# Optimization experiments

Measured on AMD Instinct MI355X. Metric: run time of the kernel, lower is better.

The kernel has to match this reference:

```python
import jax, jax.numpy as jnp
import numpy as np

E = 131072
MS, MV = 64, 32            # node/edge/out irreps: 64x0e + 32x1o (dim 160)
DIM = MS + 3 * MV
SC = 64                    # edge scalar dim
BETA = 1.6791767           # normalize2mom(silu) constant used by e3nn FullyConnectedNet
SQ3 = np.float32(np.sqrt(3.0))


def _split(x, ms, mv):
    # e3nn layout: [mul_s scalars | mul_v vectors (mul-major, xyz-minor)]
    return x[:, :ms], x[:, ms:].reshape(x.shape[0], mv, 3)


def _tp(xs, xv, ys, yv, Wss, Wvv, Wsv, Wvs):
    # uvw fully-connected tensor product of (m1s x0e + m1v x1o) with (1x0e + 1x1o),
    # component irrep normalization, 1/sqrt(fan_in) path weights.
    m1s, m1v = xs.shape[1], xv.shape[1]
    s_a = jnp.einsum('eu,uw->ew', xs * ys, Wss) / np.sqrt(m1s)              # 0e x 0e -> 0e
    dot = jnp.einsum('eui,ei->eu', xv, yv) / SQ3                            # 1o x 1o -> 0e
    s_b = jnp.einsum('eu,uw->ew', dot, Wvv) / np.sqrt(m1v)
    v_a = jnp.einsum('eu,ei,uw->ewi', xs, yv, Wsv) / np.sqrt(m1s)           # 0e x 1o -> 1o
    v_b = jnp.einsum('eui,uw->ewi', xv * ys[:, :, None], Wvs) / np.sqrt(m1v)  # 1o x 0e -> 1o
    return jnp.concatenate([s_a, s_b], 1), jnp.concatenate([v_a, v_b], 1)


def _mlp(x, W1, W2, W3):
    # e3nn FullyConnectedNet with silu: variance-preserving layers
    h = BETA * jax.nn.silu(x @ W1 / np.sqrt(W1.shape[0]))
    h = BETA * jax.nn.silu(h @ W2 / np.sqrt(W2.shape[0]))
    return h @ W3 / np.sqrt(W3.shape[0])


def _scale_linear(ms_, mv_, w, Wls, Wlv):
    # LinearScaleWithWeights: per-channel (uvu) scale by generated weights, then o3.Linear
    nS = ms_.shape[1]
    s = ms_ * w[:, :nS]
    v = mv_ * w[:, nS:, None]
    s2 = s @ Wls / np.sqrt(Wls.shape[0])
    v2 = jnp.einsum('eui,uw->ewi', v, Wlv) / np.sqrt(Wlv.shape[0])
    return s2, v2


def _linear(s, v, Ws, Wv):
    return s @ Ws / np.sqrt(Ws.shape[0]), jnp.einsum('eui,uw->ewi', v, Wv) / np.sqrt(Wv.shape[0])


def setup_inputs() -> dict:
    key = jax.random.key(0)
    ks = jax.random.split(key, 32)
    r = lambda i, shp: jax.random.normal(ks[i], shp, dtype=jnp.float32)
    return {
        'node_feats_src': r(0, (E, DIM)),
        'node_feats_dst': r(1, (E, DIM)),
        'edge_feats':     r(2, (E, DIM)),
        'local_env_edge': r(3, (E, 4)),
        'edge_scalars':   r(4, (E, SC)),
        # node TP (combined 128x0e+64x1o x 1x0e+1x1o -> 128x0e+64x1o)
        'Wn_ss': r(5, (2 * MS, MS)), 'Wn_vv': r(6, (2 * MV, MS)),
        'Wn_sv': r(7, (2 * MS, MV)), 'Wn_vs': r(8, (2 * MV, MV)),
        # edge TP (64x0e+32x1o x 1x0e+1x1o -> 128x0e+64x1o)
        'We_ss': r(9, (MS, MS)), 'We_vv': r(10, (MV, MS)),
        'We_sv': r(11, (MS, MV)), 'We_vs': r(12, (MV, MV)),
        # scaler output linears (128x0e+64x1o -> 64x0e+32x1o)
        'Wns_s': r(13, (2 * MS, MS)), 'Wns_v': r(14, (2 * MV, MV)),
        'Wes_s': r(15, (2 * MS, MS)), 'Wes_v': r(16, (2 * MV, MV)),
        # final output linears (irreps_out -> irreps_out)
        'Wno_s': r(17, (MS, MS)), 'Wno_v': r(18, (MV, MV)),
        'Weo_s': r(19, (MS, MS)), 'Weo_v': r(20, (MV, MV)),
        # radial MLPs [64,64,64,192]
        'Wnm1': r(21, (SC, 64)), 'Wnm2': r(22, (64, 64)), 'Wnm3': r(23, (64, 2 * MS + 2 * MV)),
        'Wem1': r(24, (SC, 64)), 'Wem2': r(25, (64, 64)), 'Wem3': r(26, (64, 2 * MS + 2 * MV)),
    }


def reference(node_feats_src, node_feats_dst, edge_feats, local_env_edge, edge_scalars,
              Wn_ss, Wn_vv, Wn_sv, Wn_vs, We_ss, We_vv, We_sv, We_vs,
              Wns_s, Wns_v, Wes_s, Wes_v, Wno_s, Wno_v, Weo_s, Weo_v,
              Wnm1, Wnm2, Wnm3, Wem1, Wem2, Wem3):
    ss, sv = _split(node_feats_src, MS, MV)
    ds, dv = _split(node_feats_dst, MS, MV)
    # AttentionHeadsToVector over stack([src,dst]): per-irrep concat -> 128x0e + 64x1o
    xs = jnp.concatenate([ss, ds], 1)
    xv = jnp.concatenate([sv, dv], 1)
    ys = local_env_edge[:, :1]
    yv = local_env_edge[:, 1:4]
    # node branch
    w_n = _mlp(edge_scalars, Wnm1, Wnm2, Wnm3)
    m_s, m_v = _tp(xs, xv, ys, yv, Wn_ss, Wn_vv, Wn_sv, Wn_vs)
    n_s, n_v = _scale_linear(m_s, m_v, w_n, Wns_s, Wns_v)
    # edge branch
    w_e = _mlp(edge_scalars, Wem1, Wem2, Wem3)
    es, ev = _split(edge_feats, MS, MV)
    e_ms, e_mv = _tp(es, ev, ys, yv, We_ss, We_vv, We_sv, We_vs)
    e_s, e_v = _scale_linear(e_ms, e_mv, w_e, Wes_s, Wes_v)
    # final linears + sum
    on_s, on_v = _linear(n_s, n_v, Wno_s, Wno_v)
    oe_s, oe_v = _linear(e_s, e_v, Weo_s, Weo_v)
    out_s = on_s + oe_s
    out_v = on_v + oe_v
    return jnp.concatenate([out_s, out_v.reshape(out_v.shape[0], -1)], 1)
```

## Files before the change

kernel.cpp:

```cpp
#include <hip/hip_runtime.h>


typedef short  bf16x8 __attribute__((ext_vector_type(8)));
typedef float  f32x4  __attribute__((ext_vector_type(4)));

#define FENCE() asm volatile("" ::: "memory")

constexpr float BETA  = 1.6791767f;
constexpr float RS128 = 0.088388347648318447f;
constexpr float RS64  = 0.125f;
constexpr float RS32  = 0.176776695296636881f;
constexpr float RSQ3  = 0.577350269189625842f;

enum : int {
  O_nm1 = 0,      O_nm2 = 4096,   O_nm3 = 8192,
  O_em1 = 20480,  O_em2 = 24576,  O_em3 = 28672,
  O_nss = 40960,  O_nsv = 49152,  O_nvv = 53248,  O_nvs = 57344,
  O_ess = 59392,  O_esv = 63488,  O_evv = 65536,  O_evs = 67584,
  O_cns = 68608,  O_cnv = 76800,  O_ces = 78848,  O_cev = 87040,
  W_TOTAL = 89088
};

enum : int { ST = 260, H0n = 0, H0e = 64, H1n = 128, H1e = 192, MSP = 0, MV = 128 };

struct Ptrs {
  const float *src, *dst, *ef, *env, *scal;
  const ushort* wf;
  float *out;
};

struct PrepArgs {
  const float* src[14];
  int K[14], N[14], ofs[14];
  ushort* dst;
};
struct Prep2Args {
  const float* A[4]; const float* B[4];
  int K[4], N[4], inner[4], ofs[4];
  float scale[4];
  ushort* dst;
};

__device__ __forceinline__ ushort f2b(float x) {
  union { float f; unsigned u; } v; v.f = x;
  unsigned r = v.u + 0x7fffu + ((v.u >> 16) & 1u);
  return (ushort)(r >> 16);
}
__device__ __forceinline__ unsigned pk2(float a, float b) {
  unsigned r;
  asm("v_cvt_pk_bf16_f32 %0, %1, %2" : "=v"(r) : "v"(a), "v"(b));
  return r;
}
__device__ __forceinline__ float plo(unsigned p) {
  union { unsigned u; float f; } v; v.u = p << 16; return v.f;
}
__device__ __forceinline__ float phi(unsigned p) {
  union { unsigned u; float f; } v; v.u = p & 0xffff0000u; return v.f;
}

__global__ __launch_bounds__(256) void prep_kernel(PrepArgs A) {
  const int mat = blockIdx.x;
  const float* __restrict__ src = A.src[mat];
  const int K = A.K[mat], N = A.N[mat], KS = K >> 5;
  ushort* dst = A.dst + A.ofs[mat];
  const int total = (N * K) >> 3;
  for (int gi = threadIdx.x; gi < total; gi += 256) {
    int t = gi / (64 * KS), r = gi - t * 64 * KS;
    int ks = r >> 6, lane = r & 63;
    int cc = lane & 15, gg = lane >> 4;
    int n = t * 16 + cc, k0 = ks * 32 + gg * 8;
    ushort v[8];
#pragma unroll
    for (int j = 0; j < 8; ++j) v[j] = f2b(src[(size_t)(k0 + j) * N + n]);
    *(uint4*)(dst + (size_t)gi * 8) = *(const uint4*)v;
  }
}

__global__ __launch_bounds__(256) void prep2_kernel(Prep2Args Z) {
  const int m = blockIdx.x;
  const float* __restrict__ A = Z.A[m];
  const float* __restrict__ B = Z.B[m];
  const int K = Z.K[m], N = Z.N[m], I = Z.inner[m], KS = K >> 5;
  const float sc = Z.scale[m];
  ushort* dst = Z.dst + Z.ofs[m];

  __shared__ float sAt[8192];
  __shared__ float sB [4096];
  for (int idx = threadIdx.x; idx < K * I; idx += 256) {
    int k = idx / I, u = idx - k * I;
    sAt[u * K + k] = A[idx];
  }
  for (int idx = threadIdx.x; idx < I * N; idx += 256) sB[idx] = B[idx];
  __syncthreads();

  const int total = (N * K) >> 3;
  for (int gi = blockIdx.y * 256 + threadIdx.x; gi < total; gi += gridDim.y * 256) {
    int t = gi / (64 * KS), r = gi - t * 64 * KS;
    int ks = r >> 6, lane = r & 63;
    int cc = lane & 15, gg = lane >> 4;
    int n = t * 16 + cc, k0 = ks * 32 + gg * 8;
    float acc[8] = {0, 0, 0, 0, 0, 0, 0, 0};
    for (int u = 0; u < I; ++u) {
      float bv = sB[u * N + n];
      const float* ap = &sAt[u * K + k0];
#pragma unroll
      for (int j = 0; j < 8; ++j) acc[j] += ap[j] * bv;
    }
    ushort v[8];
#pragma unroll
    for (int j = 0; j < 8; ++j) v[j] = f2b(acc[j] * sc);
    *(uint4*)(dst + (size_t)gi * 8) = *(const uint4*)v;
  }
}

template<int N>
__device__ __forceinline__ void lda(const ushort* __restrict__ wb, unsigned lofs, bf16x8* a) {
#pragma unroll
  for (int i = 0; i < N; ++i) a[i] = *(const bf16x8*)(wb + i * 512 + lofs);
}
template<int T, int KS>
__device__ __forceinline__ void mfm(const bf16x8* a, const bf16x8* bf, f32x4* out) {
#pragma unroll
  for (int t = 0; t < T; ++t) {
    f32x4 acc = (f32x4){0, 0, 0, 0};
#pragma unroll
    for (int ks = 0; ks < KS; ++ks)
      acc = __builtin_amdgcn_mfma_f32_16x16x32_bf16(a[t * KS + ks], bf[ks], acc, 0, 0, 0);
    out[t] = acc;
  }
}
template<int T, int KS>
__device__ __forceinline__ void mfmacc(const bf16x8* a, const bf16x8* bf, f32x4* out) {
#pragma unroll
  for (int t = 0; t < T; ++t)
#pragma unroll
    for (int ks = 0; ks < KS; ++ks)
      out[t] = __builtin_amdgcn_mfma_f32_16x16x32_bf16(a[t * KS + ks], bf[ks], out[t], 0, 0, 0);
}

__device__ __forceinline__ void put2(ushort* b, int cg, int col, const f32x4& d) {
  uint2 p; p.x = pk2(d[0], d[1]); p.y = pk2(d[2], d[3]);
  *(uint2*)(b + cg + col) = p;
}
__device__ __forceinline__ bf16x8 getf(const ushort* b, int cg, int col, int g) {
  return *(const bf16x8*)(b + cg + col + 8 * g);
}
__device__ __forceinline__ bf16x8 ldf8(const float* __restrict__ p) {
  float4 a = *(const float4*)p, b4 = *(const float4*)(p + 4);
  union { unsigned u[4]; bf16x8 v; } r;
  r.u[0] = pk2(a.x, a.y); r.u[1] = pk2(a.z, a.w);
  r.u[2] = pk2(b4.x, b4.y); r.u[3] = pk2(b4.z, b4.w);
  return r.v;
}
__device__ __forceinline__ f32x4 silu4(const f32x4& d) {
  f32x4 o;
#pragma unroll
  for (int r = 0; r < 4; ++r) { float z = d[r] * 0.125f; o[r] = BETA * z / (1.f + __expf(-z)); }
  return o;
}
__device__ __forceinline__ void vecwin(const float* __restrict__ p,
                                       float y0, float y1, float y2,
                                       bf16x8& dotf, bf16x8* xvf) {
  float v[24];
#pragma unroll
  for (int q = 0; q < 6; ++q) *(float4*)&v[4 * q] = *(const float4*)(p + 4 * q);
  float dj[8];
#pragma unroll
  for (int j = 0; j < 8; ++j)
    dj[j] = (v[3 * j] * y0 + v[3 * j + 1] * y1 + v[3 * j + 2] * y2) * RSQ3;
  union { unsigned u[4]; bf16x8 w; } t;
#pragma unroll
  for (int q = 0; q < 4; ++q) t.u[q] = pk2(dj[2 * q], dj[2 * q + 1]);
  dotf = t.w;
#pragma unroll
  for (int i = 0; i < 3; ++i) {
#pragma unroll
    for (int q = 0; q < 4; ++q) t.u[q] = pk2(v[6 * q + i], v[6 * q + 3 + i]);
    xvf[i] = t.w;
  }
}

__device__ __forceinline__ void mlp3(const ushort* __restrict__ wb, unsigned lofs,
                                     const bf16x8* h2, uint2* Wp) {
  bf16x8 aa[6], ab[6];
  lda<6>(wb, lofs, aa);
  lda<6>(wb + 6 * 512, lofs, ab);
  f32x4 dw[3];
  mfm<3, 2>(aa, h2, dw);
  lda<6>(wb + 12 * 512, lofs, aa);
#pragma unroll
  for (int t = 0; t < 3; ++t) { Wp[t].x = pk2(dw[t][0]*0.125f, dw[t][1]*0.125f); Wp[t].y = pk2(dw[t][2]*0.125f, dw[t][3]*0.125f); }
  mfm<3, 2>(ab, h2, dw);
  lda<6>(wb + 18 * 512, lofs, ab);
#pragma unroll
  for (int t = 0; t < 3; ++t) { Wp[3+t].x = pk2(dw[t][0]*0.125f, dw[t][1]*0.125f); Wp[3+t].y = pk2(dw[t][2]*0.125f, dw[t][3]*0.125f); }
  mfm<3, 2>(aa, h2, dw);
#pragma unroll
  for (int t = 0; t < 3; ++t) { Wp[6+t].x = pk2(dw[t][0]*0.125f, dw[t][1]*0.125f); Wp[6+t].y = pk2(dw[t][2]*0.125f, dw[t][3]*0.125f); }
  mfm<3, 2>(ab, h2, dw);
#pragma unroll
  for (int t = 0; t < 3; ++t) { Wp[9+t].x = pk2(dw[t][0]*0.125f, dw[t][1]*0.125f); Wp[9+t].y = pk2(dw[t][2]*0.125f, dw[t][3]*0.125f); }
}

template<bool ED, bool ACC>
__device__ __forceinline__ void tp_sl(
    const ushort* __restrict__ WF, ushort* bA, int cg, int g, unsigned lofs,
    const bf16x8* xsf, const bf16x8* dotf, const bf16x8* xvi,
    const uint2* Wp, float ys, float yv0, float yv1, float yv2,
    f32x4* os, f32x4 (*ov)[2]) {
  constexpr int KA = ED ? 2 : 4;
  constexpr int KB = ED ? 1 : 2;
  const float SA = ED ? RS64 : RS128;
  const float SB = ED ? RS32 : RS64;

  {
    bf16x8 a[4 * KA]; f32x4 d[4];
    lda<4 * KA>(WF + (ED ? O_ess : O_nss), lofs, a);
    mfm<4, KA>(a, xsf, d);
#pragma unroll
    for (int t = 0; t < 4; ++t) {
      f32x4 m;
      m[0] = d[t][0]*ys*SA*plo(Wp[t].x); m[1] = d[t][1]*ys*SA*phi(Wp[t].x);
      m[2] = d[t][2]*ys*SA*plo(Wp[t].y); m[3] = d[t][3]*ys*SA*phi(Wp[t].y);
      put2(bA, cg, MSP + 16 * t + 4 * g, m);
    }
  }
  {
    bf16x8 a[4 * KB]; f32x4 d[4];
    lda<4 * KB>(WF + (ED ? O_evv : O_nvv), lofs, a);
    mfm<4, KB>(a, dotf, d);
#pragma unroll
    for (int t = 0; t < 4; ++t) {
      f32x4 m;
      m[0] = d[t][0]*SB*plo(Wp[4+t].x); m[1] = d[t][1]*SB*phi(Wp[4+t].x);
      m[2] = d[t][2]*SB*plo(Wp[4+t].y); m[3] = d[t][3]*SB*phi(Wp[4+t].y);
      put2(bA, cg, MSP + 64 + 16 * t + 4 * g, m);
    }
  }
  FENCE();
  bf16x8 mpf[4];
#pragma unroll
  for (int ks = 0; ks < 4; ++ks) mpf[ks] = getf(bA, cg, MSP + 32 * ks, g);
  bf16x8 acs[16];
  lda<16>(WF + (ED ? O_ces : O_cns), lofs, acs);

  f32x4 ga[2];
  {
    bf16x8 a[2 * KA];
    lda<2 * KA>(WF + (ED ? O_esv : O_nsv), lofs, a);
    mfm<2, KA>(a, xsf, ga);
  }
  bf16x8 avs[2 * KB];
  lda<2 * KB>(WF + (ED ? O_evs : O_nvs), lofs, avs);
  bf16x8 acv[4];
  lda<4>(WF + (ED ? O_cev : O_cnv), lofs, acv);
#pragma unroll
  for (int i = 0; i < 3; ++i) {
    f32x4 db[2];
    mfm<2, KB>(avs, xvi + i * KB, db);
    float yvi = (i == 0) ? yv0 : ((i == 1) ? yv1 : yv2);
#pragma unroll
    for (int t = 0; t < 2; ++t) {
      f32x4 m;
      m[0] = ga[t][0]*SA*yvi*plo(Wp[8+t].x); m[1] = ga[t][1]*SA*yvi*phi(Wp[8+t].x);
      m[2] = ga[t][2]*SA*yvi*plo(Wp[8+t].y); m[3] = ga[t][3]*SA*yvi*phi(Wp[8+t].y);
      put2(bA, cg, MV + 16 * t + 4 * g, m);
    }
#pragma unroll
    for (int t = 0; t < 2; ++t) {
      f32x4 m;
      m[0] = db[t][0]*ys*SB*plo(Wp[10+t].x); m[1] = db[t][1]*ys*SB*phi(Wp[10+t].x);
      m[2] = db[t][2]*ys*SB*plo(Wp[10+t].y); m[3] = db[t][3]*ys*SB*phi(Wp[10+t].y);
      put2(bA, cg, MV + 32 + 16 * t + 4 * g, m);
    }
    FENCE();
    bf16x8 mvf[2] = { getf(bA, cg, MV, g), getf(bA, cg, MV + 32, g) };
    if (ACC) mfmacc<2, 2>(acv, mvf, ov[i]);
    else     mfm<2, 2>(acv, mvf, ov[i]);
    FENCE();
  }
  if (ACC) mfmacc<4, 4>(acs, mpf, os);
  else     mfm<4, 4>(acs, mpf, os);
}

__global__ __launch_bounds__(64, 2) void mp_kernel(Ptrs P) {
  const int lane = threadIdx.x & 63;
  const int c    = lane & 15, g  = lane >> 4;
  const unsigned lofs = lane * 8;
  const int cg   = c * ST;
  const int e    = blockIdx.x * 16 + c;
  const ushort* __restrict__ WF = P.wf;

  __shared__ ushort sb[16][ST];
  ushort* bA = &sb[0][0];

  const float* __restrict__ rs = P.src + (size_t)e * 160;
  const float* __restrict__ rd = P.dst + (size_t)e * 160;
  const float* __restrict__ re = P.ef  + (size_t)e * 160;
  const float* __restrict__ rq = P.scal + (size_t)e * 64;

  bf16x8 a1n[8], a1e[8];
  lda<8>(WF + O_nm1, lofs, a1n);
  lda<8>(WF + O_em1, lofs, a1e);

  float4 ev = *(const float4*)(P.env + (size_t)e * 4);
  const float ys = ev.x, yv0 = ev.y, yv1 = ev.z, yv2 = ev.w;
  bf16x8 sc[2];
  sc[0] = ldf8(rq + 8 * g);
  sc[1] = ldf8(rq + 32 + 8 * g);

  {
    f32x4 dn[4], de[4];
    mfm<4, 2>(a1n, sc, dn); mfm<4, 2>(a1e, sc, de);
#pragma unroll
    for (int t = 0; t < 4; ++t) put2(bA, cg, H0n + 16 * t + 4 * g, silu4(dn[t]));
#pragma unroll
    for (int t = 0; t < 4; ++t) put2(bA, cg, H0e + 16 * t + 4 * g, silu4(de[t]));
  }
  FENCE();

  bf16x8 a2n[8], a2e[8];
  lda<8>(WF + O_nm2, lofs, a2n);
  lda<8>(WF + O_em2, lofs, a2e);
  bf16x8 xsf_n[4];
  xsf_n[0] = ldf8(rs + 8 * g);  xsf_n[1] = ldf8(rs + 32 + 8 * g);
  xsf_n[2] = ldf8(rd + 8 * g);  xsf_n[3] = ldf8(rd + 32 + 8 * g);
  bf16x8 dot_n[2], xv_n[6];
  {
    bf16x8 tmp[3];
    vecwin(rs + 64 + 24 * g, yv0, yv1, yv2, dot_n[0], tmp);
    xv_n[0] = tmp[0]; xv_n[2] = tmp[1]; xv_n[4] = tmp[2];
    vecwin(rd + 64 + 24 * g, yv0, yv1, yv2, dot_n[1], tmp);
    xv_n[1] = tmp[0]; xv_n[3] = tmp[1]; xv_n[5] = tmp[2];
  }
  {
    bf16x8 hn[2] = { getf(bA, cg, H0n, g), getf(bA, cg, H0n + 32, g) };
    bf16x8 he[2] = { getf(bA, cg, H0e, g), getf(bA, cg, H0e + 32, g) };
    f32x4 dn[4], de[4];
    mfm<4, 2>(a2n, hn, dn); mfm<4, 2>(a2e, he, de);
#pragma unroll
    for (int t = 0; t < 4; ++t) put2(bA, cg, H1n + 16 * t + 4 * g, silu4(dn[t]));
#pragma unroll
    for (int t = 0; t < 4; ++t) put2(bA, cg, H1e + 16 * t + 4 * g, silu4(de[t]));
  }
  FENCE();

  uint2 Wpn[12];
  {
    bf16x8 h2n[2] = { getf(bA, cg, H1n, g), getf(bA, cg, H1n + 32, g) };
    mlp3(WF + O_nm3, lofs, h2n, Wpn);
  }
  FENCE();

  f32x4 os[4]; f32x4 ov[3][2];
  tp_sl<false, false>(WF, bA, cg, g, lofs, xsf_n, dot_n, xv_n, Wpn, ys, yv0, yv1, yv2, os, ov);

  bf16x8 xsf_e[2], dot_e[1], xv_e[3];
  xsf_e[0] = ldf8(re + 8 * g); xsf_e[1] = ldf8(re + 32 + 8 * g);
  {
    bf16x8 tmp[3];
    vecwin(re + 64 + 24 * g, yv0, yv1, yv2, dot_e[0], tmp);
    xv_e[0] = tmp[0]; xv_e[1] = tmp[1]; xv_e[2] = tmp[2];
  }
  uint2 Wpe[12];
  {
    bf16x8 h2e[2] = { getf(bA, cg, H1e, g), getf(bA, cg, H1e + 32, g) };
    mlp3(WF + O_em3, lofs, h2e, Wpe);
  }
  FENCE();

  tp_sl<true, true>(WF, bA, cg, g, lofs, xsf_e, dot_e, xv_e, Wpe, ys, yv0, yv1, yv2, os, ov);

  float* __restrict__ po = P.out + (size_t)e * 160;
#pragma unroll
  for (int t = 0; t < 4; ++t) {
    float4 o = { os[t][0], os[t][1], os[t][2], os[t][3] };
    *(float4*)(po + 16 * t + 4 * g) = o;
  }
#pragma unroll
  for (int t = 0; t < 2; ++t) {
    float vv[12];
#pragma unroll
    for (int r = 0; r < 4; ++r)
#pragma unroll
      for (int i = 0; i < 3; ++i) vv[3 * r + i] = ov[i][t][r];
    *(float4*)(po + 64 + 48 * t + 12 * g)     = *(float4*)&vv[0];
    *(float4*)(po + 64 + 48 * t + 12 * g + 4) = *(float4*)&vv[4];
    *(float4*)(po + 64 + 48 * t + 12 * g + 8) = *(float4*)&vv[8];
  }
}

extern "C" void kernel_launch(void* const* d_in, const int* in_sizes, int n_in,
                              void* d_out, int out_size, void* d_ws, size_t ws_size,
                              hipStream_t stream) {
  PrepArgs A;
  const int src_idx[14] = {21,22,23, 24,25,26, 5,7,6,8, 9,11,10,12};
  const int Ks[14] = {64,64,64, 64,64,64, 128,128,64,64, 64,64,32,32};
  const int Ns[14] = {64,64,192, 64,64,192, 64,32,64,32, 64,32,64,32};
  const int Os[14] = {O_nm1,O_nm2,O_nm3, O_em1,O_em2,O_em3,
                      O_nss,O_nsv,O_nvv,O_nvs, O_ess,O_esv,O_evv,O_evs};
  for (int i = 0; i < 14; ++i) {
    A.src[i] = (const float*)d_in[src_idx[i]];
    A.K[i] = Ks[i]; A.N[i] = Ns[i]; A.ofs[i] = Os[i];
  }
  A.dst = (ushort*)d_ws;
  prep_kernel<<<dim3(14), dim3(256), 0, stream>>>(A);

  Prep2Args Z;
  Z.A[0] = (const float*)d_in[13]; Z.B[0] = (const float*)d_in[17];
  Z.K[0] = 128; Z.N[0] = 64; Z.inner[0] = 64; Z.ofs[0] = O_cns; Z.scale[0] = RS128 * RS64;
  Z.A[1] = (const float*)d_in[14]; Z.B[1] = (const float*)d_in[18];
  Z.K[1] = 64;  Z.N[1] = 32; Z.inner[1] = 32; Z.ofs[1] = O_cnv; Z.scale[1] = RS64 * RS32;
  Z.A[2] = (const float*)d_in[15]; Z.B[2] = (const float*)d_in[19];
  Z.K[2] = 128; Z.N[2] = 64; Z.inner[2] = 64; Z.ofs[2] = O_ces; Z.scale[2] = RS128 * RS64;
  Z.A[3] = (const float*)d_in[16]; Z.B[3] = (const float*)d_in[20];
  Z.K[3] = 64;  Z.N[3] = 32; Z.inner[3] = 32; Z.ofs[3] = O_cev; Z.scale[3] = RS64 * RS32;
  Z.dst = (ushort*)d_ws;
  prep2_kernel<<<dim3(4, 4), dim3(256), 0, stream>>>(Z);

  Ptrs P;
  P.src  = (const float*)d_in[0];
  P.dst  = (const float*)d_in[1];
  P.ef   = (const float*)d_in[2];
  P.env  = (const float*)d_in[3];
  P.scal = (const float*)d_in[4];
  P.wf   = (const ushort*)d_ws;
  P.out  = (float*)d_out;

  const int E = in_sizes[0] / 160;
  mp_kernel<<<dim3(E / 16), dim3(64), 0, stream>>>(P);
}
```

Measured before the change: 148.6 us.

## Process two 16-edge tiles per wave to reuse weight fragments

Each 64-lane wavefront now handles 32 edges as two 16-edge tiles, A and B. Every weight fragment loaded for the MLP layers, tensor products and final linears is applied to both tiles, which halves weight-load traffic per edge. The shared buffer doubles to 32 rows and the grid halves. Some loads are split into halves to limit register pressure, but keeping two sets of accumulators and inputs live still raises register use, which risks spills or lower occupancy.

```diff
diff --git a/kernel.cpp b/kernel.cpp
--- a/kernel.cpp
+++ b/kernel.cpp
@@ -180,75 +180,84 @@
   }
 }
 
-__device__ __forceinline__ void mlp3(const ushort* __restrict__ wb, unsigned lofs,
-                                     const bf16x8* h2, uint2* Wp) {
-  bf16x8 aa[6], ab[6];
-  lda<6>(wb, lofs, aa);
-  lda<6>(wb + 6 * 512, lofs, ab);
-  f32x4 dw[3];
-  mfm<3, 2>(aa, h2, dw);
-  lda<6>(wb + 12 * 512, lofs, aa);
-#pragma unroll
-  for (int t = 0; t < 3; ++t) { Wp[t].x = pk2(dw[t][0]*0.125f, dw[t][1]*0.125f); Wp[t].y = pk2(dw[t][2]*0.125f, dw[t][3]*0.125f); }
-  mfm<3, 2>(ab, h2, dw);
-  lda<6>(wb + 18 * 512, lofs, ab);
-#pragma unroll
-  for (int t = 0; t < 3; ++t) { Wp[3+t].x = pk2(dw[t][0]*0.125f, dw[t][1]*0.125f); Wp[3+t].y = pk2(dw[t][2]*0.125f, dw[t][3]*0.125f); }
-  mfm<3, 2>(aa, h2, dw);
-#pragma unroll
-  for (int t = 0; t < 3; ++t) { Wp[6+t].x = pk2(dw[t][0]*0.125f, dw[t][1]*0.125f); Wp[6+t].y = pk2(dw[t][2]*0.125f, dw[t][3]*0.125f); }
-  mfm<3, 2>(ab, h2, dw);
-#pragma unroll
-  for (int t = 0; t < 3; ++t) { Wp[9+t].x = pk2(dw[t][0]*0.125f, dw[t][1]*0.125f); Wp[9+t].y = pk2(dw[t][2]*0.125f, dw[t][3]*0.125f); }
+__device__ __forceinline__ void mlp3_2(const ushort* __restrict__ wb, unsigned lofs,
+                                       const bf16x8* h2A, const bf16x8* h2B,
+                                       uint2* WpA, uint2* WpB) {
+#pragma unroll
+  for (int q = 0; q < 4; ++q) {
+    bf16x8 a[6];
+    lda<6>(wb + q * 6 * 512, lofs, a);
+    f32x4 dw[3];
+    mfm<3, 2>(a, h2A, dw);
+#pragma unroll
+    for (int t = 0; t < 3; ++t) {
+      WpA[q*3+t].x = pk2(dw[t][0]*0.125f, dw[t][1]*0.125f);
+      WpA[q*3+t].y = pk2(dw[t][2]*0.125f, dw[t][3]*0.125f);
+    }
+    mfm<3, 2>(a, h2B, dw);
+#pragma unroll
+    for (int t = 0; t < 3; ++t) {
+      WpB[q*3+t].x = pk2(dw[t][0]*0.125f, dw[t][1]*0.125f);
+      WpB[q*3+t].y = pk2(dw[t][2]*0.125f, dw[t][3]*0.125f);
+    }
+  }
 }
 
 template<bool ED, bool ACC>
-__device__ __forceinline__ void tp_sl(
-    const ushort* __restrict__ WF, ushort* bA, int cg, int g, unsigned lofs,
-    const bf16x8* xsf, const bf16x8* dotf, const bf16x8* xvi,
-    const uint2* Wp, float ys, float yv0, float yv1, float yv2,
-    f32x4* os, f32x4 (*ov)[2]) {
+__device__ __forceinline__ void tp_sl2(
+    const ushort* __restrict__ WF, ushort* bA, int cgA, int cgB, int g, unsigned lofs,
+    const bf16x8* xsfA, const bf16x8* xsfB,
+    const bf16x8* dotA, const bf16x8* dotB,
+    const bf16x8* xvA,  const bf16x8* xvB,
+    const uint2* WpA, const uint2* WpB,
+    float ysA, float ysB,
+    float yvA0, float yvA1, float yvA2,
+    float yvB0, float yvB1, float yvB2,
+    f32x4* osA, f32x4* osB, f32x4 (*ovA)[2], f32x4 (*ovB)[2]) {
   constexpr int KA = ED ? 2 : 4;
   constexpr int KB = ED ? 1 : 2;
   const float SA = ED ? RS64 : RS128;
   const float SB = ED ? RS32 : RS64;
 
-  {
-    bf16x8 a[4 * KA]; f32x4 d[4];
-    lda<4 * KA>(WF + (ED ? O_ess : O_nss), lofs, a);
-    mfm<4, KA>(a, xsf, d);
+#pragma unroll
+  for (int half = 0; half < 2; ++half) {
+    bf16x8 a[2 * KA];
+    lda<2 * KA>(WF + (ED ? O_ess : O_nss) + half * 2 * KA * 512, lofs, a);
+    f32x4 dA[2], dB[2];
+    mfm<2, KA>(a, xsfA, dA); mfm<2, KA>(a, xsfB, dB);
+#pragma unroll
+    for (int t = 0; t < 2; ++t) {
+      int tt = half * 2 + t;
+      f32x4 m;
+      m[0] = dA[t][0]*ysA*SA*plo(WpA[tt].x); m[1] = dA[t][1]*ysA*SA*phi(WpA[tt].x);
+      m[2] = dA[t][2]*ysA*SA*plo(WpA[tt].y); m[3] = dA[t][3]*ysA*SA*phi(WpA[tt].y);
+      put2(bA, cgA, MSP + 16 * tt + 4 * g, m);
+      m[0] = dB[t][0]*ysB*SA*plo(WpB[tt].x); m[1] = dB[t][1]*ysB*SA*phi(WpB[tt].x);
+      m[2] = dB[t][2]*ysB*SA*plo(WpB[tt].y); m[3] = dB[t][3]*ysB*SA*phi(WpB[tt].y);
+      put2(bA, cgB, MSP + 16 * tt + 4 * g, m);
+    }
+  }
+  {
+    bf16x8 a[4 * KB];
+    lda<4 * KB>(WF + (ED ? O_evv : O_nvv), lofs, a);
+    f32x4 dA[4], dB[4];
+    mfm<4, KB>(a, dotA, dA); mfm<4, KB>(a, dotB, dB);
 #pragma unroll
     for (int t = 0; t < 4; ++t) {
       f32x4 m;
-      m[0] = d[t][0]*ys*SA*plo(Wp[t].x); m[1] = d[t][1]*ys*SA*phi(Wp[t].x);
-      m[2] = d[t][2]*ys*SA*plo(Wp[t].y); m[3] = d[t][3]*ys*SA*phi(Wp[t].y);
-      put2(bA, cg, MSP + 16 * t + 4 * g, m);
-    }
-  }
-  {
-    bf16x8 a[4 * KB]; f32x4 d[4];
-    lda<4 * KB>(WF + (ED ? O_evv : O_nvv), lofs, a);
-    mfm<4, KB>(a, dotf, d);
-#pragma unroll
-    for (int t = 0; t < 4; ++t) {
-      f32x4 m;
-      m[0] = d[t][0]*SB*plo(Wp[4+t].x); m[1] = d[t][1]*SB*phi(Wp[4+t].x);
-      m[2] = d[t][2]*SB*plo(Wp[4+t].y); m[3] = d[t][3]*SB*phi(Wp[4+t].y);
-      put2(bA, cg, MSP + 64 + 16 * t + 4 * g, m);
-    }
-  }
-  FENCE();
-  bf16x8 mpf[4];
-#pragma unroll
-  for (int ks = 0; ks < 4; ++ks) mpf[ks] = getf(bA, cg, MSP + 32 * ks, g);
-  bf16x8 acs[16];
-  lda<16>(WF + (ED ? O_ces : O_cns), lofs, acs);
-
-  f32x4 ga[2];
+      m[0] = dA[t][0]*SB*plo(WpA[4+t].x); m[1] = dA[t][1]*SB*phi(WpA[4+t].x);
+      m[2] = dA[t][2]*SB*plo(WpA[4+t].y); m[3] = dA[t][3]*SB*phi(WpA[4+t].y);
+      put2(bA, cgA, MSP + 64 + 16 * t + 4 * g, m);
+      m[0] = dB[t][0]*SB*plo(WpB[4+t].x); m[1] = dB[t][1]*SB*phi(WpB[4+t].x);
+      m[2] = dB[t][2]*SB*plo(WpB[4+t].y); m[3] = dB[t][3]*SB*phi(WpB[4+t].y);
+      put2(bA, cgB, MSP + 64 + 16 * t + 4 * g, m);
+    }
+  }
+  f32x4 gaA[2], gaB[2];
   {
     bf16x8 a[2 * KA];
     lda<2 * KA>(WF + (ED ? O_esv : O_nsv), lofs, a);
-    mfm<2, KA>(a, xsf, ga);
+    mfm<2, KA>(a, xsfA, gaA); mfm<2, KA>(a, xsfB, gaB);
   }
   bf16x8 avs[2 * KB];
   lda<2 * KB>(WF + (ED ? O_evs : O_nvs), lofs, avs);
@@ -256,137 +265,215 @@
   lda<4>(WF + (ED ? O_cev : O_cnv), lofs, acv);
 #pragma unroll
   for (int i = 0; i < 3; ++i) {
-    f32x4 db[2];
-    mfm<2, KB>(avs, xvi + i * KB, db);
-    float yvi = (i == 0) ? yv0 : ((i == 1) ? yv1 : yv2);
+    f32x4 dbA[2], dbB[2];
+    mfm<2, KB>(avs, xvA + i * KB, dbA);
+    mfm<2, KB>(avs, xvB + i * KB, dbB);
+    float yviA = (i == 0) ? yvA0 : ((i == 1) ? yvA1 : yvA2);
+    float yviB = (i == 0) ? yvB0 : ((i == 1) ? yvB1 : yvB2);
 #pragma unroll
     for (int t = 0; t < 2; ++t) {
       f32x4 m;
-      m[0] = ga[t][0]*SA*yvi*plo(Wp[8+t].x); m[1] = ga[t][1]*SA*yvi*phi(Wp[8+t].x);
-      m[2] = ga[t][2]*SA*yvi*plo(Wp[8+t].y); m[3] = ga[t][3]*SA*yvi*phi(Wp[8+t].y);
-      put2(bA, cg, MV + 16 * t + 4 * g, m);
+      m[0] = gaA[t][0]*SA*yviA*plo(WpA[8+t].x); m[1] = gaA[t][1]*SA*yviA*phi(WpA[8+t].x);
+      m[2] = gaA[t][2]*SA*yviA*plo(WpA[8+t].y); m[3] = gaA[t][3]*SA*yviA*phi(WpA[8+t].y);
+      put2(bA, cgA, MV + 16 * t + 4 * g, m);
+      m[0] = gaB[t][0]*SA*yviB*plo(WpB[8+t].x); m[1] = gaB[t][1]*SA*yviB*phi(WpB[8+t].x);
+      m[2] = gaB[t][2]*SA*yviB*plo(WpB[8+t].y); m[3] = gaB[t][3]*SA*yviB*phi(WpB[8+t].y);
+      put2(bA, cgB, MV + 16 * t + 4 * g, m);
     }
 #pragma unroll
     for (int t = 0; t < 2; ++t) {
       f32x4 m;
-      m[0] = db[t][0]*ys*SB*plo(Wp[10+t].x); m[1] = db[t][1]*ys*SB*phi(Wp[10+t].x);
-      m[2] = db[t][2]*ys*SB*plo(Wp[10+t].y); m[3] = db[t][3]*ys*SB*phi(Wp[10+t].y);
-      put2(bA, cg, MV + 32 + 16 * t + 4 * g, m);
+      m[0] = dbA[t][0]*ysA*SB*plo(WpA[10+t].x); m[1] = dbA[t][1]*ysA*SB*phi(WpA[10+t].x);
+      m[2] = dbA[t][2]*ysA*SB*plo(WpA[10+t].y); m[3] = dbA[t][3]*ysA*SB*phi(WpA[10+t].y);
+      put2(bA, cgA, MV + 32 + 16 * t + 4 * g, m);
+      m[0] = dbB[t][0]*ysB*SB*plo(WpB[10+t].x); m[1] = dbB[t][1]*ysB*SB*phi(WpB[10+t].x);
+      m[2] = dbB[t][2]*ysB*SB*plo(WpB[10+t].y); m[3] = dbB[t][3]*ysB*SB*phi(WpB[10+t].y);
+      put2(bA, cgB, MV + 32 + 16 * t + 4 * g, m);
     }
     FENCE();
-    bf16x8 mvf[2] = { getf(bA, cg, MV, g), getf(bA, cg, MV + 32, g) };
-    if (ACC) mfmacc<2, 2>(acv, mvf, ov[i]);
-    else     mfm<2, 2>(acv, mvf, ov[i]);
+    bf16x8 mvfA[2] = { getf(bA, cgA, MV, g), getf(bA, cgA, MV + 32, g) };
+    bf16x8 mvfB[2] = { getf(bA, cgB, MV, g), getf(bA, cgB, MV + 32, g) };
+    if (ACC) { mfmacc<2, 2>(acv, mvfA, ovA[i]); mfmacc<2, 2>(acv, mvfB, ovB[i]); }
+    else     { mfm<2, 2>(acv, mvfA, ovA[i]);    mfm<2, 2>(acv, mvfB, ovB[i]); }
     FENCE();
   }
-  if (ACC) mfmacc<4, 4>(acs, mpf, os);
-  else     mfm<4, 4>(acs, mpf, os);
+  bf16x8 mpfA[4], mpfB[4];
+#pragma unroll
+  for (int ks = 0; ks < 4; ++ks) {
+    mpfA[ks] = getf(bA, cgA, MSP + 32 * ks, g);
+    mpfB[ks] = getf(bA, cgB, MSP + 32 * ks, g);
+  }
+#pragma unroll
+  for (int h = 0; h < 2; ++h) {
+    bf16x8 a[8];
+    lda<8>(WF + (ED ? O_ces : O_cns) + h * 8 * 512, lofs, a);
+    if (ACC) { mfmacc<2, 4>(a, mpfA, osA + 2 * h); mfmacc<2, 4>(a, mpfB, osB + 2 * h); }
+    else     { mfm<2, 4>(a, mpfA, osA + 2 * h);    mfm<2, 4>(a, mpfB, osB + 2 * h); }
+  }
 }
 
 __global__ __launch_bounds__(64, 2) void mp_kernel(Ptrs P) {
   const int lane = threadIdx.x & 63;
   const int c    = lane & 15, g  = lane >> 4;
   const unsigned lofs = lane * 8;
-  const int cg   = c * ST;
-  const int e    = blockIdx.x * 16 + c;
+  const int cgA  = c * ST;
+  const int cgB  = (c + 16) * ST;
+  const int eA   = blockIdx.x * 32 + c;
+  const int eB   = eA + 16;
   const ushort* __restrict__ WF = P.wf;
 
-  __shared__ ushort sb[16][ST];
+  __shared__ ushort sb[32][ST];
   ushort* bA = &sb[0][0];
 
-  const float* __restrict__ rs = P.src + (size_t)e * 160;
-  const float* __restrict__ rd = P.dst + (size_t)e * 160;
-  const float* __restrict__ re = P.ef  + (size_t)e * 160;
-  const float* __restrict__ rq = P.scal + (size_t)e * 64;
-
-  bf16x8 a1n[8], a1e[8];
-  lda<8>(WF + O_nm1, lofs, a1n);
-  lda<8>(WF + O_em1, lofs, a1e);
-
-  float4 ev = *(const float4*)(P.env + (size_t)e * 4);
-  const float ys = ev.x, yv0 = ev.y, yv1 = ev.z, yv2 = ev.w;
-  bf16x8 sc[2];
-  sc[0] = ldf8(rq + 8 * g);
-  sc[1] = ldf8(rq + 32 + 8 * g);
-
-  {
-    f32x4 dn[4], de[4];
-    mfm<4, 2>(a1n, sc, dn); mfm<4, 2>(a1e, sc, de);
-#pragma unroll
-    for (int t = 0; t < 4; ++t) put2(bA, cg, H0n + 16 * t + 4 * g, silu4(dn[t]));
-#pragma unroll
-    for (int t = 0; t < 4; ++t) put2(bA, cg, H0e + 16 * t + 4 * g, silu4(de[t]));
+  const float* __restrict__ rsA = P.src + (size_t)eA * 160;
+  const float* __restrict__ rdA = P.dst + (size_t)eA * 160;
+  const float* __restrict__ reA = P.ef  + (size_t)eA * 160;
+  const float* __restrict__ rqA = P.scal + (size_t)eA * 64;
+  const float* __restrict__ rsB = P.src + (size_t)eB * 160;
+  const float* __restrict__ rdB = P.dst + (size_t)eB * 160;
+  const float* __restrict__ reB = P.ef  + (size_t)eB * 160;
+  const float* __restrict__ rqB = P.scal + (size_t)eB * 64;
+
+  float4 evA = *(const float4*)(P.env + (size_t)eA * 4);
+  float4 evB = *(const float4*)(P.env + (size_t)eB * 4);
+  const float ysA = evA.x, yvA0 = evA.y, yvA1 = evA.z, yvA2 = evA.w;
+  const float ysB = evB.x, yvB0 = evB.y, yvB1 = evB.z, yvB2 = evB.w;
+
+  {
+    bf16x8 a1n[8], a1e[8];
+    lda<8>(WF + O_nm1, lofs, a1n);
+    lda<8>(WF + O_em1, lofs, a1e);
+    bf16x8 scA[2], scB[2];
+    scA[0] = ldf8(rqA + 8 * g); scA[1] = ldf8(rqA + 32 + 8 * g);
+    scB[0] = ldf8(rqB + 8 * g); scB[1] = ldf8(rqB + 32 + 8 * g);
+    f32x4 d[4];
+    mfm<4, 2>(a1n, scA, d);
+#pragma unroll
+    for (int t = 0; t < 4; ++t) put2(bA, cgA, H0n + 16 * t + 4 * g, silu4(d[t]));
+    mfm<4, 2>(a1n, scB, d);
+#pragma unroll
+    for (int t = 0; t < 4; ++t) put2(bA, cgB, H0n + 16 * t + 4 * g, silu4(d[t]));
+    mfm<4, 2>(a1e, scA, d);
+#pragma unroll
+    for (int t = 0; t < 4; ++t) put2(bA, cgA, H0e + 16 * t + 4 * g, silu4(d[t]));
+    mfm<4, 2>(a1e, scB, d);
+#pragma unroll
+    for (int t = 0; t < 4; ++t) put2(bA, cgB, H0e + 16 * t + 4 * g, silu4(d[t]));
   }
   FENCE();
 
-  bf16x8 a2n[8], a2e[8];
-  lda<8>(WF + O_nm2, lofs, a2n);
-  lda<8>(WF + O_em2, lofs, a2e);
-  bf16x8 xsf_n[4];
-  xsf_n[0] = ldf8(rs + 8 * g);  xsf_n[1] = ldf8(rs + 32 + 8 * g);
-  xsf_n[2] = ldf8(rd + 8 * g);  xsf_n[3] = ldf8(rd + 32 + 8 * g);
-  bf16x8 dot_n[2], xv_n[6];
+  bf16x8 xsf_nA[4], xsf_nB[4];
+  xsf_nA[0] = ldf8(rsA + 8 * g);  xsf_nA[1] = ldf8(rsA + 32 + 8 * g);
+  xsf_nA[2] = ldf8(rdA + 8 * g);  xsf_nA[3] = ldf8(rdA + 32 + 8 * g);
+  xsf_nB[0] = ldf8(rsB + 8 * g);  xsf_nB[1] = ldf8(rsB + 32 + 8 * g);
+  xsf_nB[2] = ldf8(rdB + 8 * g);  xsf_nB[3] = ldf8(rdB + 32 + 8 * g);
+  bf16x8 dot_nA[2], xv_nA[6], dot_nB[2], xv_nB[6];
   {
     bf16x8 tmp[3];
-    vecwin(rs + 64 + 24 * g, yv0, yv1, yv2, dot_n[0], tmp);
-    xv_n[0] = tmp[0]; xv_n[2] = tmp[1]; xv_n[4] = tmp[2];
-    vecwin(rd + 64 + 24 * g, yv0, yv1, yv2, dot_n[1], tmp);
-    xv_n[1] = tmp[0]; xv_n[3] = tmp[1]; xv_n[5] = tmp[2];
-  }
-  {
-    bf16x8 hn[2] = { getf(bA, cg, H0n, g), getf(bA, cg, H0n + 32, g) };
-    bf16x8 he[2] = { getf(bA, cg, H0e, g), getf(bA, cg, H0e + 32, g) };
-    f32x4 dn[4], de[4];
-    mfm<4, 2>(a2n, hn, dn); mfm<4, 2>(a2e, he, de);
-#pragma unroll
-    for (int t = 0; t < 4; ++t) put2(bA, cg, H1n + 16 * t + 4 * g, silu4(dn[t]));
-#pragma unroll
-    for (int t = 0; t < 4; ++t) put2(bA, cg, H1e + 16 * t + 4 * g, silu4(de[t]));
+    vecwin(rsA + 64 + 24 * g, yvA0, yvA1, yvA2, dot_nA[0], tmp);
+    xv_nA[0] = tmp[0]; xv_nA[2] = tmp[1]; xv_nA[4] = tmp[2];
+    vecwin(rdA + 64 + 24 * g, yvA0, yvA1, yvA2, dot_nA[1], tmp);
+    xv_nA[1] = tmp[0]; xv_nA[3] = tmp[1]; xv_nA[5] = tmp[2];
+    vecwin(rsB + 64 + 24 * g, yvB0, yvB1, yvB2, dot_nB[0], tmp);
+    xv_nB[0] = tmp[0]; xv_nB[2] = tmp[1]; xv_nB[4] = tmp[2];
+    vecwin(rdB + 64 + 24 * g, yvB0, yvB1, yvB2, dot_nB[1], tmp);
+    xv_nB[1] = tmp[0]; xv_nB[3] = tmp[1]; xv_nB[5] = tmp[2];
+  }
+
+  {
+    bf16x8 a2[8];
+    lda<8>(WF + O_nm2, lofs, a2);
+    bf16x8 hA[2] = { getf(bA, cgA, H0n, g), getf(bA, cgA, H0n + 32, g) };
+    bf16x8 hB[2] = { getf(bA, cgB, H0n, g), getf(bA, cgB, H0n + 32, g) };
+    f32x4 d[4];
+    mfm<4, 2>(a2, hA, d);
+#pragma unroll
+    for (int t = 0; t < 4; ++t) put2(bA, cgA, H1n + 16 * t + 4 * g, silu4(d[t]));
+    mfm<4, 2>(a2, hB, d);
+#pragma unroll
+    for (int t = 0; t < 4; ++t) put2(bA, cgB, H1n + 16 * t + 4 * g, silu4(d[t]));
+    lda<8>(WF + O_em2, lofs, a2);
+    hA[0] = getf(bA, cgA, H0e, g); hA[1] = getf(bA, cgA, H0e + 32, g);
+    hB[0] = getf(bA, cgB, H0e, g); hB[1] = getf(bA, cgB, H0e + 32, g);
+    mfm<4, 2>(a2, hA, d);
+#pragma unroll
+    for (int t = 0; t < 4; ++t) put2(bA, cgA, H1e + 16 * t + 4 * g, silu4(d[t]));
+    mfm<4, 2>(a2, hB, d);
+#pragma unroll
+    for (int t = 0; t < 4; ++t) put2(bA, cgB, H1e + 16 * t + 4 * g, silu4(d[t]));
   }
   FENCE();
 
-  uint2 Wpn[12];
-  {
-    bf16x8 h2n[2] = { getf(bA, cg, H1n, g), getf(bA, cg, H1n + 32, g) };
-    mlp3(WF + O_nm3, lofs, h2n, Wpn);
+  uint2 WpnA[12], WpnB[12];
+  {
+    bf16x8 h2A[2] = { getf(bA, cgA, H1n, g), getf(bA, cgA, H1n + 32, g) };
+    bf16x8 h2B[2] = { getf(bA, cgB, H1n, g), getf(bA, cgB, H1n + 32, g) };
+    mlp3_2(WF + O_nm3, lofs, h2A, h2B, WpnA, WpnB);
   }
   FENCE();
 
-  f32x4 os[4]; f32x4 ov[3][2];
-  tp_sl<false, false>(WF, bA, cg, g, lofs, xsf_n, dot_n, xv_n, Wpn, ys, yv0, yv1, yv2, os, ov);
-
-  bf16x8 xsf_e[2], dot_e[1], xv_e[3];
-  xsf_e[0] = ldf8(re + 8 * g); xsf_e[1] = ldf8(re + 32 + 8 * g);
-  {
-    bf16x8 tmp[3];
-    vecwin(re + 64 + 24 * g, yv0, yv1, yv2, dot_e[0], tmp);
-    xv_e[0] = tmp[0]; xv_e[1] = tmp[1]; xv_e[2] = tmp[2];
-  }
-  uint2 Wpe[12];
-  {
-    bf16x8 h2e[2] = { getf(bA, cg, H1e, g), getf(bA, cg, H1e + 32, g) };
-    mlp3(WF + O_em3, lofs, h2e, Wpe);
+  f32x4 osA[4], osB[4]; f32x4 ovA[3][2], ovB[3][2];
+  tp_sl2<false, false>(WF, bA, cgA, cgB, g, lofs,
+                       xsf_nA, xsf_nB, dot_nA, dot_nB, xv_nA, xv_nB,
+                       WpnA, WpnB, ysA, ysB, yvA0, yvA1, yvA2, yvB0, yvB1, yvB2,
+                       osA, osB, ovA, ovB);
+
+  uint2 WpeA[12], WpeB[12];
+  {
+    bf16x8 h2A[2] = { getf(bA, cgA, H1e, g), getf(bA, cgA, H1e + 32, g) };
+    bf16x8 h2B[2] = { getf(bA, cgB, H1e, g), getf(bA, cgB, H1e + 32, g) };
+    mlp3_2(WF + O_em3, lofs, h2A, h2B, WpeA, WpeB);
   }
   FENCE();
 
-  tp_sl<true, true>(WF, bA, cg, g, lofs, xsf_e, dot_e, xv_e, Wpe, ys, yv0, yv1, yv2, os, ov);
-
-  float* __restrict__ po = P.out + (size_t)e * 160;
-#pragma unroll
-  for (int t = 0; t < 4; ++t) {
-    float4 o = { os[t][0], os[t][1], os[t][2], os[t][3] };
-    *(float4*)(po + 16 * t + 4 * g) = o;
-  }
-#pragma unroll
-  for (int t = 0; t < 2; ++t) {
-    float vv[12];
-#pragma unroll
-    for (int r = 0; r < 4; ++r)
-#pragma unroll
-      for (int i = 0; i < 3; ++i) vv[3 * r + i] = ov[i][t][r];
-    *(float4*)(po + 64 + 48 * t + 12 * g)     = *(float4*)&vv[0];
-    *(float4*)(po + 64 + 48 * t + 12 * g + 4) = *(float4*)&vv[4];
-    *(float4*)(po + 64 + 48 * t + 12 * g + 8) = *(float4*)&vv[8];
+  bf16x8 xsf_eA[2], xsf_eB[2], dot_eA[1], dot_eB[1], xv_eA[3], xv_eB[3];
+  xsf_eA[0] = ldf8(reA + 8 * g); xsf_eA[1] = ldf8(reA + 32 + 8 * g);
+  xsf_eB[0] = ldf8(reB + 8 * g); xsf_eB[1] = ldf8(reB + 32 + 8 * g);
+  vecwin(reA + 64 + 24 * g, yvA0, yvA1, yvA2, dot_eA[0], xv_eA);
+  vecwin(reB + 64 + 24 * g, yvB0, yvB1, yvB2, dot_eB[0], xv_eB);
+
+  tp_sl2<true, true>(WF, bA, cgA, cgB, g, lofs,
+                     xsf_eA, xsf_eB, dot_eA, dot_eB, xv_eA, xv_eB,
+                     WpeA, WpeB, ysA, ysB, yvA0, yvA1, yvA2, yvB0, yvB1, yvB2,
+                     osA, osB, ovA, ovB);
+
+  {
+    float* __restrict__ po = P.out + (size_t)eA * 160;
+#pragma unroll
+    for (int t = 0; t < 4; ++t) {
+      float4 o = { osA[t][0], osA[t][1], osA[t][2], osA[t][3] };
+      *(float4*)(po + 16 * t + 4 * g) = o;
+    }
+#pragma unroll
+    for (int t = 0; t < 2; ++t) {
+      float vv[12];
+#pragma unroll
+      for (int r = 0; r < 4; ++r)
+#pragma unroll
+        for (int i = 0; i < 3; ++i) vv[3 * r + i] = ovA[i][t][r];
+      *(float4*)(po + 64 + 48 * t + 12 * g)     = *(float4*)&vv[0];
+      *(float4*)(po + 64 + 48 * t + 12 * g + 4) = *(float4*)&vv[4];
+      *(float4*)(po + 64 + 48 * t + 12 * g + 8) = *(float4*)&vv[8];
+    }
+  }
+  {
+    float* __restrict__ po = P.out + (size_t)eB * 160;
+#pragma unroll
+    for (int t = 0; t < 4; ++t) {
+      float4 o = { osB[t][0], osB[t][1], osB[t][2], osB[t][3] };
+      *(float4*)(po + 16 * t + 4 * g) = o;
+    }
+#pragma unroll
+    for (int t = 0; t < 2; ++t) {
+      float vv[12];
+#pragma unroll
+      for (int r = 0; r < 4; ++r)
+#pragma unroll
+        for (int i = 0; i < 3; ++i) vv[3 * r + i] = ovB[i][t][r];
+      *(float4*)(po + 64 + 48 * t + 12 * g)     = *(float4*)&vv[0];
+      *(float4*)(po + 64 + 48 * t + 12 * g + 4) = *(float4*)&vv[4];
+      *(float4*)(po + 64 + 48 * t + 12 * g + 8) = *(float4*)&vv[8];
+    }
   }
 }
 
@@ -428,5 +515,5 @@
   P.out  = (float*)d_out;
 
   const int E = in_sizes[0] / 160;
-  mp_kernel<<<dim3(E / 16), dim3(64), 0, stream>>>(P);
-}
+  mp_kernel<<<dim3(E / 32), dim3(64), 0, stream>>>(P);
+}
```

Measured after the change: 138.9 us. 1.07x faster.

## Split fused node/edge kernel into two per-branch launches accumulating into output

Applied to the files above, without the earlier changes.

Splits the single kernel that computed both the node and edge branches into two templated launches. The node pass writes the output and the edge pass reads it back and adds its own result. This halves the live weight fragments and shared scratch per wave, which is meant to cut register pressure and allow more concurrency. In exchange it adds an extra global read and write of the output, a second launch, and repeats the env loads.

```diff
diff --git a/kernel.cpp b/kernel.cpp
--- a/kernel.cpp
+++ b/kernel.cpp
@@ -21,7 +21,7 @@
   W_TOTAL = 89088
 };
 
-enum : int { ST = 260, H0n = 0, H0e = 64, H1n = 128, H1e = 192, MSP = 0, MV = 128 };
+enum : int { ST = 196, H0 = 0, H1 = 64, MSP = 0, MV = 128 };
 
 struct Ptrs {
   const float *src, *dst, *ef, *env, *scal;
@@ -129,14 +129,6 @@
     out[t] = acc;
   }
 }
-template<int T, int KS>
-__device__ __forceinline__ void mfmacc(const bf16x8* a, const bf16x8* bf, f32x4* out) {
-#pragma unroll
-  for (int t = 0; t < T; ++t)
-#pragma unroll
-    for (int ks = 0; ks < KS; ++ks)
-      out[t] = __builtin_amdgcn_mfma_f32_16x16x32_bf16(a[t * KS + ks], bf[ks], out[t], 0, 0, 0);
-}
 
 __device__ __forceinline__ void put2(ushort* b, int cg, int col, const f32x4& d) {
   uint2 p; p.x = pk2(d[0], d[1]); p.y = pk2(d[2], d[3]);
@@ -182,27 +174,21 @@
 
 __device__ __forceinline__ void mlp3(const ushort* __restrict__ wb, unsigned lofs,
                                      const bf16x8* h2, uint2* Wp) {
-  bf16x8 aa[6], ab[6];
-  lda<6>(wb, lofs, aa);
-  lda<6>(wb + 6 * 512, lofs, ab);
-  f32x4 dw[3];
-  mfm<3, 2>(aa, h2, dw);
-  lda<6>(wb + 12 * 512, lofs, aa);
-#pragma unroll
-  for (int t = 0; t < 3; ++t) { Wp[t].x = pk2(dw[t][0]*0.125f, dw[t][1]*0.125f); Wp[t].y = pk2(dw[t][2]*0.125f, dw[t][3]*0.125f); }
-  mfm<3, 2>(ab, h2, dw);
-  lda<6>(wb + 18 * 512, lofs, ab);
-#pragma unroll
-  for (int t = 0; t < 3; ++t) { Wp[3+t].x = pk2(dw[t][0]*0.125f, dw[t][1]*0.125f); Wp[3+t].y = pk2(dw[t][2]*0.125f, dw[t][3]*0.125f); }
-  mfm<3, 2>(aa, h2, dw);
-#pragma unroll
-  for (int t = 0; t < 3; ++t) { Wp[6+t].x = pk2(dw[t][0]*0.125f, dw[t][1]*0.125f); Wp[6+t].y = pk2(dw[t][2]*0.125f, dw[t][3]*0.125f); }
-  mfm<3, 2>(ab, h2, dw);
-#pragma unroll
-  for (int t = 0; t < 3; ++t) { Wp[9+t].x = pk2(dw[t][0]*0.125f, dw[t][1]*0.125f); Wp[9+t].y = pk2(dw[t][2]*0.125f, dw[t][3]*0.125f); }
-}
-
-template<bool ED, bool ACC>
+#pragma unroll
+  for (int q = 0; q < 4; ++q) {
+    bf16x8 a[6];
+    lda<6>(wb + q * 6 * 512, lofs, a);
+    f32x4 dw[3];
+    mfm<3, 2>(a, h2, dw);
+#pragma unroll
+    for (int t = 0; t < 3; ++t) {
+      Wp[q*3+t].x = pk2(dw[t][0]*0.125f, dw[t][1]*0.125f);
+      Wp[q*3+t].y = pk2(dw[t][2]*0.125f, dw[t][3]*0.125f);
+    }
+  }
+}
+
+template<bool ED>
 __device__ __forceinline__ void tp_sl(
     const ushort* __restrict__ WF, ushort* bA, int cg, int g, unsigned lofs,
     const bf16x8* xsf, const bf16x8* dotf, const bf16x8* xvi,
@@ -241,8 +227,6 @@
   bf16x8 mpf[4];
 #pragma unroll
   for (int ks = 0; ks < 4; ++ks) mpf[ks] = getf(bA, cg, MSP + 32 * ks, g);
-  bf16x8 acs[16];
-  lda<16>(WF + (ED ? O_ces : O_cns), lofs, acs);
 
   f32x4 ga[2];
   {
@@ -275,15 +259,18 @@
     }
     FENCE();
     bf16x8 mvf[2] = { getf(bA, cg, MV, g), getf(bA, cg, MV + 32, g) };
-    if (ACC) mfmacc<2, 2>(acv, mvf, ov[i]);
-    else     mfm<2, 2>(acv, mvf, ov[i]);
+    mfm<2, 2>(acv, mvf, ov[i]);
     FENCE();
   }
-  if (ACC) mfmacc<4, 4>(acs, mpf, os);
-  else     mfm<4, 4>(acs, mpf, os);
-}
-
-__global__ __launch_bounds__(64, 2) void mp_kernel(Ptrs P) {
+  {
+    bf16x8 a[16];
+    lda<16>(WF + (ED ? O_ces : O_cns), lofs, a);
+    mfm<4, 4>(a, mpf, os);
+  }
+}
+
+template<bool ED>
+__global__ __launch_bounds__(64, 2) void mp_path(Ptrs P) {
   const int lane = threadIdx.x & 63;
   const int c    = lane & 15, g  = lane >> 4;
   const unsigned lofs = lane * 8;
@@ -294,99 +281,111 @@
   __shared__ ushort sb[16][ST];
   ushort* bA = &sb[0][0];
 
-  const float* __restrict__ rs = P.src + (size_t)e * 160;
-  const float* __restrict__ rd = P.dst + (size_t)e * 160;
-  const float* __restrict__ re = P.ef  + (size_t)e * 160;
+  const float* __restrict__ ra = (ED ? P.ef : P.src) + (size_t)e * 160;
+  const float* __restrict__ rb = P.dst + (size_t)e * 160;
   const float* __restrict__ rq = P.scal + (size_t)e * 64;
-
-  bf16x8 a1n[8], a1e[8];
-  lda<8>(WF + O_nm1, lofs, a1n);
-  lda<8>(WF + O_em1, lofs, a1e);
+  float* __restrict__ po = P.out + (size_t)e * 160;
 
   float4 ev = *(const float4*)(P.env + (size_t)e * 4);
   const float ys = ev.x, yv0 = ev.y, yv1 = ev.z, yv2 = ev.w;
-  bf16x8 sc[2];
-  sc[0] = ldf8(rq + 8 * g);
-  sc[1] = ldf8(rq + 32 + 8 * g);
-
-  {
-    f32x4 dn[4], de[4];
-    mfm<4, 2>(a1n, sc, dn); mfm<4, 2>(a1e, sc, de);
-#pragma unroll
-    for (int t = 0; t < 4; ++t) put2(bA, cg, H0n + 16 * t + 4 * g, silu4(dn[t]));
-#pragma unroll
-    for (int t = 0; t < 4; ++t) put2(bA, cg, H0e + 16 * t + 4 * g, silu4(de[t]));
+
+  {
+    bf16x8 a1[8];
+    lda<8>(WF + (ED ? O_em1 : O_nm1), lofs, a1);
+    bf16x8 sc[2];
+    sc[0] = ldf8(rq + 8 * g); sc[1] = ldf8(rq + 32 + 8 * g);
+    f32x4 d[4];
+    mfm<4, 2>(a1, sc, d);
+#pragma unroll
+    for (int t = 0; t < 4; ++t) put2(bA, cg, H0 + 16 * t + 4 * g, silu4(d[t]));
   }
   FENCE();
 
-  bf16x8 a2n[8], a2e[8];
-  lda<8>(WF + O_nm2, lofs, a2n);
-  lda<8>(WF + O_em2, lofs, a2e);
-  bf16x8 xsf_n[4];
-  xsf_n[0] = ldf8(rs + 8 * g);  xsf_n[1] = ldf8(rs + 32 + 8 * g);
-  xsf_n[2] = ldf8(rd + 8 * g);  xsf_n[3] = ldf8(rd + 32 + 8 * g);
-  bf16x8 dot_n[2], xv_n[6];
-  {
+  bf16x8 xsf[ED ? 2 : 4];
+  xsf[0] = ldf8(ra + 8 * g); xsf[1] = ldf8(ra + 32 + 8 * g);
+  if (!ED) { xsf[2] = ldf8(rb + 8 * g); xsf[3] = ldf8(rb + 32 + 8 * g); }
+  bf16x8 dotf[ED ? 1 : 2], xv[ED ? 3 : 6];
+  if (!ED) {
     bf16x8 tmp[3];
-    vecwin(rs + 64 + 24 * g, yv0, yv1, yv2, dot_n[0], tmp);
-    xv_n[0] = tmp[0]; xv_n[2] = tmp[1]; xv_n[4] = tmp[2];
-    vecwin(rd + 64 + 24 * g, yv0, yv1, yv2, dot_n[1], tmp);
-    xv_n[1] = tmp[0]; xv_n[3] = tmp[1]; xv_n[5] = tmp[2];
-  }
-  {
-    bf16x8 hn[2] = { getf(bA, cg, H0n, g), getf(bA, cg, H0n + 32, g) };
-    bf16x8 he[2] = { getf(bA, cg, H0e, g), getf(bA, cg, H0e + 32, g) };
-    f32x4 dn[4], de[4];
-    mfm<4, 2>(a2n, hn, dn); mfm<4, 2>(a2e, he, de);
-#pragma unroll
-    for (int t = 0; t < 4; ++t) put2(bA, cg, H1n + 16 * t + 4 * g, silu4(dn[t]));
-#pragma unroll
-    for (int t = 0; t < 4; ++t) put2(bA, cg, H1e + 16 * t + 4 * g, silu4(de[t]));
+    vecwin(ra + 64 + 24 * g, yv0, yv1, yv2, dotf[0], tmp);
+    xv[0] = tmp[0]; xv[2] = tmp[1]; xv[4] = tmp[2];
+    vecwin(rb + 64 + 24 * g, yv0, yv1, yv2, dotf[1], tmp);
+    xv[1] = tmp[0]; xv[3] = tmp[1]; xv[5] = tmp[2];
+  } else {
+    vecwin(ra + 64 + 24 * g, yv0, yv1, yv2, dotf[0], xv);
+  }
+
+  {
+    bf16x8 a2[8];
+    lda<8>(WF + (ED ? O_em2 : O_nm2), lofs, a2);
+    bf16x8 h[2] = { getf(bA, cg, H0, g), getf(bA, cg, H0 + 32, g) };
+    f32x4 d[4];
+    mfm<4, 2>(a2, h, d);
+#pragma unroll
+    for (int t = 0; t < 4; ++t) put2(bA, cg, H1 + 16 * t + 4 * g, silu4(d[t]));
   }
   FENCE();
 
-  uint2 Wpn[12];
-  {
-    bf16x8 h2n[2] = { getf(bA, cg, H1n, g), getf(bA, cg, H1n + 32, g) };
-    mlp3(WF + O_nm3, lofs, h2n, Wpn);
+  uint2 Wp[12];
+  {
+    bf16x8 h2[2] = { getf(bA, cg, H1, g), getf(bA, cg, H1 + 32, g) };
+    mlp3(WF + (ED ? O_em3 : O_nm3), lofs, h2, Wp);
   }
   FENCE();
 
+  float4 pvs[4], pvv[6];
+  if (ED) {
+#pragma unroll
+    for (int t = 0; t < 4; ++t) pvs[t] = *(const float4*)(po + 16 * t + 4 * g);
+#pragma unroll
+    for (int t = 0; t < 2; ++t)
+#pragma unroll
+      for (int q = 0; q < 3; ++q)
+        pvv[t * 3 + q] = *(const float4*)(po + 64 + 48 * t + 12 * g + 4 * q);
+  }
+
   f32x4 os[4]; f32x4 ov[3][2];
-  tp_sl<false, false>(WF, bA, cg, g, lofs, xsf_n, dot_n, xv_n, Wpn, ys, yv0, yv1, yv2, os, ov);
-
-  bf16x8 xsf_e[2], dot_e[1], xv_e[3];
-  xsf_e[0] = ldf8(re + 8 * g); xsf_e[1] = ldf8(re + 32 + 8 * g);
-  {
-    bf16x8 tmp[3];
-    vecwin(re + 64 + 24 * g, yv0, yv1, yv2, dot_e[0], tmp);
-    xv_e[0] = tmp[0]; xv_e[1] = tmp[1]; xv_e[2] = tmp[2];
-  }
-  uint2 Wpe[12];
-  {
-    bf16x8 h2e[2] = { getf(bA, cg, H1e, g), getf(bA, cg, H1e + 32, g) };
-    mlp3(WF + O_em3, lofs, h2e, Wpe);
-  }
-  FENCE();
-
-  tp_sl<true, true>(WF, bA, cg, g, lofs, xsf_e, dot_e, xv_e, Wpe, ys, yv0, yv1, yv2, os, ov);
-
-  float* __restrict__ po = P.out + (size_t)e * 160;
-#pragma unroll
-  for (int t = 0; t < 4; ++t) {
-    float4 o = { os[t][0], os[t][1], os[t][2], os[t][3] };
-    *(float4*)(po + 16 * t + 4 * g) = o;
-  }
-#pragma unroll
-  for (int t = 0; t < 2; ++t) {
-    float vv[12];
-#pragma unroll
-    for (int r = 0; r < 4; ++r)
-#pragma unroll
-      for (int i = 0; i < 3; ++i) vv[3 * r + i] = ov[i][t][r];
-    *(float4*)(po + 64 + 48 * t + 12 * g)     = *(float4*)&vv[0];
-    *(float4*)(po + 64 + 48 * t + 12 * g + 4) = *(float4*)&vv[4];
-    *(float4*)(po + 64 + 48 * t + 12 * g + 8) = *(float4*)&vv[8];
+  tp_sl<ED>(WF, bA, cg, g, lofs, xsf, dotf, xv, Wp, ys, yv0, yv1, yv2, os, ov);
+
+  if (!ED) {
+#pragma unroll
+    for (int t = 0; t < 4; ++t) {
+      float4 o = { os[t][0], os[t][1], os[t][2], os[t][3] };
+      *(float4*)(po + 16 * t + 4 * g) = o;
+    }
+#pragma unroll
+    for (int t = 0; t < 2; ++t) {
+      float vv[12];
+#pragma unroll
+      for (int r = 0; r < 4; ++r)
+#pragma unroll
+        for (int i = 0; i < 3; ++i) vv[3 * r + i] = ov[i][t][r];
+      *(float4*)(po + 64 + 48 * t + 12 * g)     = *(float4*)&vv[0];
+      *(float4*)(po + 64 + 48 * t + 12 * g + 4) = *(float4*)&vv[4];
+      *(float4*)(po + 64 + 48 * t + 12 * g + 8) = *(float4*)&vv[8];
+    }
+  } else {
+#pragma unroll
+    for (int t = 0; t < 4; ++t) {
+      float4 o = { pvs[t].x + os[t][0], pvs[t].y + os[t][1],
+                   pvs[t].z + os[t][2], pvs[t].w + os[t][3] };
+      *(float4*)(po + 16 * t + 4 * g) = o;
+    }
+#pragma unroll
+    for (int t = 0; t < 2; ++t) {
+      float vv[12];
+#pragma unroll
+      for (int r = 0; r < 4; ++r)
+#pragma unroll
+        for (int i = 0; i < 3; ++i) vv[3 * r + i] = ov[i][t][r];
+#pragma unroll
+      for (int q = 0; q < 3; ++q) {
+        float4 p = pvv[t * 3 + q];
+        float4 o = { p.x + vv[4 * q], p.y + vv[4 * q + 1],
+                     p.z + vv[4 * q + 2], p.w + vv[4 * q + 3] };
+        *(float4*)(po + 64 + 48 * t + 12 * g + 4 * q) = o;
+      }
+    }
   }
 }
 
@@ -428,5 +427,6 @@
   P.out  = (float*)d_out;
 
   const int E = in_sizes[0] / 160;
-  mp_kernel<<<dim3(E / 16), dim3(64), 0, stream>>>(P);
-}
+  mp_path<false><<<dim3(E / 16), dim3(64), 0, stream>>>(P);
+  mp_path<true ><<<dim3(E / 16), dim3(64), 0, stream>>>(P);
+}
```

Result: slower. 166.8 us (+12.3%).
